# Kernel tuning notes

Measured on AMD Instinct MI355X. Metric: run time of the kernel, lower is better.

Reference implementation:

```python
import jax, jax.numpy as jnp
import numpy as np

N_NODES = 100000
NEG_SLOPE = 0.2


def gat_conv(x, edge_index, W, a_src, a_dst, bias):
    """PyG GATConv, heads=1, concat, add_self_loops=True."""
    N = x.shape[0]
    loop = jnp.arange(N, dtype=edge_index.dtype)
    src = jnp.concatenate([edge_index[0], loop])  # message sources j
    dst = jnp.concatenate([edge_index[1], loop])  # message targets i
    h = x @ W                                      # [N, out]
    asrc = h @ a_src                               # [N]
    adst = h @ a_dst                               # [N]
    e = jax.nn.leaky_relu(asrc[src] + adst[dst], NEG_SLOPE)   # [E+N]
    m = jax.ops.segment_max(e, dst, num_segments=N)           # per-dst max
    w = jnp.exp(e - jax.lax.stop_gradient(m)[dst])
    denom = jax.ops.segment_sum(w, dst, num_segments=N)
    alpha = w / denom[dst]                                     # softmax per dst
    out = jax.ops.segment_sum(alpha[:, None] * h[src], dst, num_segments=N)
    return out + bias


def setup_inputs() -> dict:
    key = jax.random.key(0)
    ks = jax.random.split(key, 16)
    N, E, D = N_NODES, 3200000, 128
    x = jax.random.normal(ks[0], (N, D), dtype=jnp.float32)
    edge_index = jax.random.randint(ks[1], (2, E), 0, N, dtype=jnp.int64)
    def glorot(k, shape):
        fan = sum(shape)
        return jax.random.uniform(k, shape, jnp.float32, -1.0, 1.0) * np.sqrt(6.0 / fan)
    return {
        "x": x,
        "edge_index": edge_index,
        "W1": glorot(ks[2], (D, 16)),
        "a1_src": glorot(ks[3], (16,)),
        "a1_dst": glorot(ks[4], (16,)),
        "b1": jnp.zeros((16,), jnp.float32),
        "W2": glorot(ks[5], (16, 10)),
        "a2_src": glorot(ks[6], (10,)),
        "a2_dst": glorot(ks[7], (10,)),
        "b2": jnp.zeros((10,), jnp.float32),
        "Wl1": glorot(ks[8], (10, 10)),
        "bl1": jnp.zeros((10,), jnp.float32),
        "Wl2": glorot(ks[9], (10, 1)),
        "bl2": jnp.zeros((1,), jnp.float32),
    }


def reference(x, edge_index, W1, a1_src, a1_dst, b1, W2, a2_src, a2_dst, b2,
              Wl1, bl1, Wl2, bl2):
    h = gat_conv(x, edge_index, W1, a1_src, a1_dst, b1)
    h = jax.nn.relu(h)
    h = gat_conv(h, edge_index, W2, a2_src, a2_dst, b2)
    h = h @ Wl1 + bl1
    h = jax.nn.relu(h)
    return h @ Wl2 + bl2  # [N, 1]
```

## Files before the change

kernel.cpp:

```cpp
#include <hip/hip_runtime.h>
#include <hip/hip_fp16.h>


#define NEG 0.2f
#define FSH 7
#define BNODES 128
#define NSBMAX 1024
#define CAPB 4608
#define TILE 4096
#define EPT 16
#define HN 64
#define SCAP 3072
#define PESA 18

__device__ __forceinline__ float lrelu(float x) { return x > 0.0f ? x : NEG * x; }

__device__ __forceinline__ unsigned fenc(float f) {
    unsigned u = __float_as_uint(f);
    return (u & 0x80000000u) ? ~u : (u | 0x80000000u);
}
__device__ __forceinline__ float fdec(unsigned e) {
    return (e & 0x80000000u) ? __uint_as_float(e & 0x7FFFFFFFu) : __uint_as_float(~e);
}

__device__ __forceinline__ float4 ldh4(const __half* h, size_t off) {
    uint2 u = *(const uint2*)(h + off);
    __half2 a = *(__half2*)&u.x, b = *(__half2*)&u.y;
    float2 fa = __half22float2(a), fb = __half22float2(b);
    return make_float4(fa.x, fa.y, fb.x, fb.y);
}

__global__ __launch_bounds__(256) void k_front(
    const float* __restrict__ x, const float* __restrict__ W1,
    const float* __restrict__ a1s, const float* __restrict__ a1d,
    __half* __restrict__ h1, float* __restrict__ s1, float* __restrict__ d1,
    unsigned* __restrict__ gmax,
    const int* __restrict__ esrc, const int* __restrict__ edst,
    int* __restrict__ bcur, unsigned* __restrict__ pairs,
    int N, int E, int NG, int NC, int NSB)
{
    __shared__ float smem[9220];
    int tid = threadIdx.x;
    int bid = blockIdx.x;
    long long T = (long long)NG + NC;
    int before = (int)(((long long)bid * NC) / T);
    int isc = (int)((((long long)bid + 1) * NC) / T) > before;

    if (isc) {
        unsigned* lsrt = (unsigned*)smem;
        int* lhist = (int*)smem + TILE;
        int* lofs  = lhist + NSBMAX;
        int* gbase = lofs + NSBMAX;
        int* wsum  = gbase + NSBMAX;
        unsigned short* rid = (unsigned short*)(smem + TILE + 3 * NSBMAX + 4);
        int cid = before;
        int base = cid * TILE;
        int tcnt = min(TILE, E - base);
        for (int i = tid; i < NSB; i += 256) lhist[i] = 0;
        __syncthreads();
        int ed[EPT];
#pragma unroll
        for (int u = 0; u < EPT; ++u) {
            int i = tid + u * 256;
            ed[u] = (i < tcnt) ? edst[base + i] : -1;
            if (ed[u] >= 0) atomicAdd(&lhist[ed[u] >> FSH], 1);
        }
        __syncthreads();
        int i0 = 4 * tid;
        int a0 = (i0 + 0 < NSB) ? lhist[i0 + 0] : 0;
        int a1 = (i0 + 1 < NSB) ? lhist[i0 + 1] : 0;
        int a2 = (i0 + 2 < NSB) ? lhist[i0 + 2] : 0;
        int a3 = (i0 + 3 < NSB) ? lhist[i0 + 3] : 0;
        int s = a0 + a1 + a2 + a3, pfx = s;
#pragma unroll
        for (int off = 1; off < 64; off <<= 1) {
            int t = __shfl_up(pfx, off, 64);
            if ((tid & 63) >= off) pfx += t;
        }
        if ((tid & 63) == 63) wsum[tid >> 6] = pfx;
        __syncthreads();
        int carry = 0;
        for (int w = 0; w < (tid >> 6); ++w) carry += wsum[w];
        int excl = pfx + carry - s;
        if (i0 + 0 < NSB) { lofs[i0 + 0] = excl;                 gbase[i0 + 0] = a0 ? atomicAdd(&bcur[(i0 + 0) * 16], a0) : 0; }
        if (i0 + 1 < NSB) { lofs[i0 + 1] = excl + a0;            gbase[i0 + 1] = a1 ? atomicAdd(&bcur[(i0 + 1) * 16], a1) : 0; }
        if (i0 + 2 < NSB) { lofs[i0 + 2] = excl + a0 + a1;       gbase[i0 + 2] = a2 ? atomicAdd(&bcur[(i0 + 2) * 16], a2) : 0; }
        if (i0 + 3 < NSB) { lofs[i0 + 3] = excl + a0 + a1 + a2;  gbase[i0 + 3] = a3 ? atomicAdd(&bcur[(i0 + 3) * 16], a3) : 0; }
        __syncthreads();
        if (i0 + 0 < NSB) lhist[i0 + 0] = lofs[i0 + 0];
        if (i0 + 1 < NSB) lhist[i0 + 1] = lofs[i0 + 1];
        if (i0 + 2 < NSB) lhist[i0 + 2] = lofs[i0 + 2];
        if (i0 + 3 < NSB) lhist[i0 + 3] = lofs[i0 + 3];
        __syncthreads();
#pragma unroll
        for (int u = 0; u < EPT; ++u) {
            int i = tid + u * 256;
            if (ed[u] >= 0) {
                int d = ed[u], srcv = esrc[base + i];
                int b = d >> FSH;
                int pos = atomicAdd(&lhist[b], 1);
                lsrt[pos] = ((unsigned)(d & (BNODES - 1)) << 17) | (unsigned)srcv;
                rid[pos] = (unsigned short)b;
            }
        }
        __syncthreads();
        for (int i = tid; i < tcnt; i += 256) {
            int r = rid[i];
            int rel = gbase[r] + (i - lofs[r]);
            if (rel < CAPB) pairs[(size_t)r * CAPB + rel] = lsrt[i];
        }
        return;
    }

    float* sW = smem;
    float* wm = smem + 2060;
    int gid = bid - before;
    for (int i = tid; i < 2048; i += 256) sW[i + ((i >> 9) << 2)] = W1[i];
    int node0 = gid * 64;
    int node = node0 + (tid >> 2);
    int q = tid & 3;
    bool valid = node < N;
    float4 xr[8];
    {
        const float4* xp = (const float4*)x + (size_t)node * 32 + q * 8;
#pragma unroll
        for (int k = 0; k < 8; ++k)
            xr[k] = valid ? xp[k] : make_float4(0.f, 0.f, 0.f, 0.f);
    }
    __syncthreads();

    float acc[16];
#pragma unroll
    for (int c = 0; c < 16; ++c) acc[c] = 0.f;
    int wbase = q * 516;
#pragma unroll
    for (int k = 0; k < 8; ++k) {
        float xs0 = xr[k].x, xs1 = xr[k].y, xs2 = xr[k].z, xs3 = xr[k].w;
#pragma unroll
        for (int t = 0; t < 4; ++t) {
            float xv = (t == 0) ? xs0 : (t == 1) ? xs1 : (t == 2) ? xs2 : xs3;
            const float4* wrow = (const float4*)&sW[wbase + (k * 4 + t) * 16];
            float4 w0 = wrow[0], w1 = wrow[1], w2 = wrow[2], w3 = wrow[3];
            acc[0]  += xv * w0.x; acc[1]  += xv * w0.y; acc[2]  += xv * w0.z; acc[3]  += xv * w0.w;
            acc[4]  += xv * w1.x; acc[5]  += xv * w1.y; acc[6]  += xv * w1.z; acc[7]  += xv * w1.w;
            acc[8]  += xv * w2.x; acc[9]  += xv * w2.y; acc[10] += xv * w2.z; acc[11] += xv * w2.w;
            acc[12] += xv * w3.x; acc[13] += xv * w3.y; acc[14] += xv * w3.z; acc[15] += xv * w3.w;
        }
    }
#pragma unroll
    for (int c = 0; c < 16; ++c) {
        acc[c] += __shfl_xor(acc[c], 1);
        acc[c] += __shfl_xor(acc[c], 2);
    }
    float sv = 0.f, dv = 0.f;
    {
        const float4* asp = (const float4*)a1s;
        const float4* adp = (const float4*)a1d;
#pragma unroll
        for (int r = 0; r < 4; ++r) {
            float4 as = asp[r], ad = adp[r];
            sv += acc[r*4+0]*as.x + acc[r*4+1]*as.y + acc[r*4+2]*as.z + acc[r*4+3]*as.w;
            dv += acc[r*4+0]*ad.x + acc[r*4+1]*ad.y + acc[r*4+2]*ad.z + acc[r*4+3]*ad.w;
        }
    }
    if (valid) {
        float4 av;
        if      (q == 0) av = make_float4(acc[0],  acc[1],  acc[2],  acc[3]);
        else if (q == 1) av = make_float4(acc[4],  acc[5],  acc[6],  acc[7]);
        else if (q == 2) av = make_float4(acc[8],  acc[9],  acc[10], acc[11]);
        else             av = make_float4(acc[12], acc[13], acc[14], acc[15]);
        __half2 p0 = __floats2half2_rn(av.x, av.y);
        __half2 p1 = __floats2half2_rn(av.z, av.w);
        uint2 u; u.x = *(unsigned*)&p0; u.y = *(unsigned*)&p1;
        *(uint2*)&h1[(size_t)node * 16 + q * 4] = u;
        if (q == 0) { s1[node] = sv; d1[node] = dv; }
    }
    float m = valid ? sv : -3.4e38f;
#pragma unroll
    for (int off = 32; off >= 1; off >>= 1) m = fmaxf(m, __shfl_xor(m, off));
    if ((tid & 63) == 0) wm[tid >> 6] = m;
    __syncthreads();
    if (tid == 0) {
        float b = fmaxf(fmaxf(wm[0], wm[1]), fmaxf(wm[2], wm[3]));
        atomicMax(gmax, fenc(b));
    }
}

__global__ __launch_bounds__(256) void k_agg1(
    const int* __restrict__ bcur, const unsigned* __restrict__ pairs,
    const int* __restrict__ esrc, const int* __restrict__ edst,
    const float* __restrict__ s1, const float* __restrict__ d1, const __half* __restrict__ h1,
    const float* __restrict__ b1, const float* __restrict__ W2,
    const float* __restrict__ a2s, const float* __restrict__ a2d,
    __half* __restrict__ h2, float* __restrict__ s2, float* __restrict__ d2,
    const unsigned* __restrict__ gmax1p, unsigned* __restrict__ gmax2, int N, int E)
{
    __shared__ unsigned srt[SCAP];
    __shared__ float accs[HN * 17];
    __shared__ int lcnt[HN];
    __shared__ int lofs[HN + 1];
    __shared__ float dds[HN], mbs[HN];
    __shared__ float sW[160], sb[16], sas[16], sad[16];
    __shared__ float wm[4];

    int tid = threadIdx.x;
    int fb = blockIdx.x >> 1;
    int hf = blockIdx.x & 1;
    int node0 = blockIdx.x << 6;
    if (tid < 160) sW[tid] = W2[tid];
    if (tid < 16) {
        sb[tid]  = b1[tid];
        sas[tid] = (tid < 10) ? a2s[tid] : 0.f;
        sad[tid] = (tid < 10) ? a2d[tid] : 0.f;
    }
    float g0 = fdec(*gmax1p);
    if (tid < HN) {
        int n = node0 + tid;
        float dd = (n < N) ? d1[n] : 0.f;
        dds[tid] = dd; mbs[tid] = lrelu(g0 + dd);
        lcnt[tid] = 0;
    }
    __syncthreads();

    int rbase = fb * CAPB;
    int cnt = bcur[fb * 16];
    int gg = tid >> 2, q = tid & 3;

    bool ok = (cnt <= CAPB);
    unsigned pe[PESA];
    if (ok) {
#pragma unroll
        for (int u = 0; u < PESA; ++u) {
            int i = tid + u * 256;
            bool v = (i < cnt);
            pe[u] = v ? pairs[rbase + i] : 0u;
            if (v) {
                int dl = (pe[u] >> 17) & (BNODES - 1);
                if ((dl >> 6) == hf) atomicAdd(&lcnt[dl & (HN - 1)], 1);
            }
        }
        __syncthreads();
        if (tid < HN) {
            int c = lcnt[tid];
            int pfx = c;
#pragma unroll
            for (int off = 1; off < 64; off <<= 1) {
                int t = __shfl_up(pfx, off, 64);
                if (tid >= off) pfx += t;
            }
            lofs[tid + 1] = pfx;
            lcnt[tid] = pfx - c;
            if (tid == 0) lofs[0] = 0;
        }
        __syncthreads();
        if (lofs[HN] > SCAP) ok = false;
    }

    if (ok) {
#pragma unroll
        for (int u = 0; u < PESA; ++u) {
            int i = tid + u * 256;
            if (i < cnt) {
                unsigned p = pe[u];
                int dl = (p >> 17) & (BNODES - 1);
                if ((dl >> 6) == hf) {
                    int pos = atomicAdd(&lcnt[dl & (HN - 1)], 1);
                    srt[pos] = p & 0x1FFFF;
                }
            }
        }
        __syncthreads();

        int n = node0 + gg;
        float4 accv; float den;
        if (n < N) {
            float w = __expf(lrelu(s1[n] + dds[gg]) - mbs[gg]);
            float4 hv = ldh4(h1, (size_t)n * 16 + 4 * q);
            accv = make_float4(w * hv.x, w * hv.y, w * hv.z, w * hv.w);
            den = w;
        } else { accv = make_float4(0.f, 0.f, 0.f, 0.f); den = 0.f; }
        {
            float dd = dds[gg], mb = mbs[gg];
            int j = lofs[gg], j1 = lofs[gg + 1];
            for (; j + 4 <= j1; j += 4) {
                int e0 = srt[j], e1 = srt[j + 1], e2 = srt[j + 2], e3 = srt[j + 3];
                float4 H0 = ldh4(h1, (size_t)e0 * 16 + 4 * q);
                float4 H1 = ldh4(h1, (size_t)e1 * 16 + 4 * q);
                float4 H2 = ldh4(h1, (size_t)e2 * 16 + 4 * q);
                float4 H3 = ldh4(h1, (size_t)e3 * 16 + 4 * q);
                int eq = srt[j + q];
                float wq = __expf(lrelu(s1[eq] + dd) - mb);
                float w0 = __shfl(wq, 0, 4), w1 = __shfl(wq, 1, 4);
                float w2 = __shfl(wq, 2, 4), w3 = __shfl(wq, 3, 4);
                accv.x += w0 * H0.x + w1 * H1.x + w2 * H2.x + w3 * H3.x;
                accv.y += w0 * H0.y + w1 * H1.y + w2 * H2.y + w3 * H3.y;
                accv.z += w0 * H0.z + w1 * H1.z + w2 * H2.z + w3 * H3.z;
                accv.w += w0 * H0.w + w1 * H1.w + w2 * H2.w + w3 * H3.w;
                den += (w0 + w1) + (w2 + w3);
            }
            for (; j < j1; ++j) {
                int e0 = srt[j];
                float w0 = __expf(lrelu(s1[e0] + dd) - mb);
                float4 H0 = ldh4(h1, (size_t)e0 * 16 + 4 * q);
                accv.x += w0 * H0.x; accv.y += w0 * H0.y;
                accv.z += w0 * H0.z; accv.w += w0 * H0.w;
                den += w0;
            }
        }
        accs[gg * 17 + 4 * q + 0] = accv.x;
        accs[gg * 17 + 4 * q + 1] = accv.y;
        accs[gg * 17 + 4 * q + 2] = accv.z;
        accs[gg * 17 + 4 * q + 3] = accv.w;
        if (q == 0) accs[gg * 17 + 16] = den;
        __syncthreads();
    } else {
        for (int i = tid; i < HN * 17; i += 256) accs[i] = 0.f;
        __syncthreads();
        if (tid < HN) {
            int n = node0 + tid;
            if (n < N) {
                float w = __expf(lrelu(s1[n] + dds[tid]) - mbs[tid]);
#pragma unroll
                for (int t = 0; t < 16; ++t)
                    accs[tid * 17 + t] = w * __half2float(h1[(size_t)n * 16 + t]);
                accs[tid * 17 + 16] = w;
            }
        }
        __syncthreads();
        for (int i = tid; i < E; i += 256) {
            int d = edst[i];
            if ((d >> 6) != blockIdx.x) continue;
            int nl = d & (HN - 1), src = esrc[i];
            float w = __expf(lrelu(s1[src] + dds[nl]) - mbs[nl]);
#pragma unroll
            for (int t = 0; t < 16; ++t)
                atomicAdd(&accs[nl * 17 + t], w * __half2float(h1[(size_t)src * 16 + t]));
            atomicAdd(&accs[nl * 17 + 16], w);
        }
        __syncthreads();
    }

    int g = tid >> 4, k = tid & 15;
    float sval = -3.4e38f;
#pragma unroll
    for (int qq = 0; qq < 4; ++qq) {
        int nl = g * 4 + qq, nn = node0 + nl;
        if (nn >= N) continue;
        float inv = 1.f / accs[nl * 17 + 16];
        float o = fmaxf(accs[nl * 17 + k] * inv + sb[k], 0.f);
        float hh = 0.f;
#pragma unroll
        for (int kk = 0; kk < 16; ++kk) {
            float ov = __shfl(o, kk, 16);
            if (k < 10) hh += ov * sW[kk * 10 + k];
        }
        if (k >= 10) hh = 0.f;
        float ts = hh * sas[k];
        float td = hh * sad[k];
#pragma unroll
        for (int off = 1; off < 16; off <<= 1) {
            ts += __shfl_xor(ts, off, 16);
            td += __shfl_xor(td, off, 16);
        }
        h2[(size_t)nn * 16 + k] = __float2half_rn(hh);
        if (k == 0) { s2[nn] = ts; d2[nn] = td; }
        sval = fmaxf(sval, ts);
    }
    float m = sval;
#pragma unroll
    for (int off = 32; off >= 1; off >>= 1) m = fmaxf(m, __shfl_xor(m, off));
    if ((tid & 63) == 0) wm[tid >> 6] = m;
    __syncthreads();
    if (tid == 0) {
        float bmx = fmaxf(fmaxf(wm[0], wm[1]), fmaxf(wm[2], wm[3]));
        atomicMax(gmax2, fenc(bmx));
    }
}

__global__ __launch_bounds__(256) void k_agg2(
    const int* __restrict__ bcur, const unsigned* __restrict__ pairs,
    const int* __restrict__ esrc, const int* __restrict__ edst,
    const float* __restrict__ s2, const float* __restrict__ d2, const __half* __restrict__ h2,
    const float* __restrict__ b2, const float* __restrict__ Wl1, const float* __restrict__ bl1,
    const float* __restrict__ Wl2, const float* __restrict__ bl2,
    const unsigned* __restrict__ gmax2p, float* __restrict__ out, int N, int E)
{
    __shared__ unsigned srt[SCAP];
    __shared__ float accs[HN * 17];
    __shared__ int lcnt[HN];
    __shared__ int lofs[HN + 1];
    __shared__ float dds[HN], mbs[HN];
    __shared__ float sW1[100], sb1[16], sW2[16], sb2g[16];
    __shared__ float sbl2;

    int tid = threadIdx.x;
    int fb = blockIdx.x >> 1;
    int hf = blockIdx.x & 1;
    int node0 = blockIdx.x << 6;
    if (tid < 100) sW1[tid] = Wl1[tid];
    if (tid < 16) {
        sb1[tid]  = (tid < 10) ? bl1[tid] : 0.f;
        sW2[tid]  = (tid < 10) ? Wl2[tid] : 0.f;
        sb2g[tid] = (tid < 10) ? b2[tid]  : 0.f;
    }
    if (tid == 0) sbl2 = bl2[0];
    float g0 = fdec(*gmax2p);
    if (tid < HN) {
        int n = node0 + tid;
        float dd = (n < N) ? d2[n] : 0.f;
        dds[tid] = dd; mbs[tid] = lrelu(g0 + dd);
        lcnt[tid] = 0;
    }
    __syncthreads();

    int rbase = fb * CAPB;
    int cnt = bcur[fb * 16];
    int gg = tid >> 2, q = tid & 3;

    bool ok = (cnt <= CAPB);
    unsigned pe[PESA];
    if (ok) {
#pragma unroll
        for (int u = 0; u < PESA; ++u) {
            int i = tid + u * 256;
            bool v = (i < cnt);
            pe[u] = v ? pairs[rbase + i] : 0u;
            if (v) {
                int dl = (pe[u] >> 17) & (BNODES - 1);
                if ((dl >> 6) == hf) atomicAdd(&lcnt[dl & (HN - 1)], 1);
            }
        }
        __syncthreads();
        if (tid < HN) {
            int c = lcnt[tid];
            int pfx = c;
#pragma unroll
            for (int off = 1; off < 64; off <<= 1) {
                int t = __shfl_up(pfx, off, 64);
                if (tid >= off) pfx += t;
            }
            lofs[tid + 1] = pfx;
            lcnt[tid] = pfx - c;
            if (tid == 0) lofs[0] = 0;
        }
        __syncthreads();
        if (lofs[HN] > SCAP) ok = false;
    }

    if (ok) {
#pragma unroll
        for (int u = 0; u < PESA; ++u) {
            int i = tid + u * 256;
            if (i < cnt) {
                unsigned p = pe[u];
                int dl = (p >> 17) & (BNODES - 1);
                if ((dl >> 6) == hf) {
                    int pos = atomicAdd(&lcnt[dl & (HN - 1)], 1);
                    srt[pos] = p & 0x1FFFF;
                }
            }
        }
        __syncthreads();

        int n = node0 + gg;
        float4 accv; float den;
        if (n < N) {
            float w = __expf(lrelu(s2[n] + dds[gg]) - mbs[gg]);
            float4 hv = ldh4(h2, (size_t)n * 16 + 4 * q);
            accv = make_float4(w * hv.x, w * hv.y, w * hv.z, w * hv.w);
            den = w;
        } else { accv = make_float4(0.f, 0.f, 0.f, 0.f); den = 0.f; }
        {
            float dd = dds[gg], mb = mbs[gg];
            int j = lofs[gg], j1 = lofs[gg + 1];
            for (; j + 4 <= j1; j += 4) {
                int e0 = srt[j], e1 = srt[j + 1], e2 = srt[j + 2], e3 = srt[j + 3];
                float4 H0 = ldh4(h2, (size_t)e0 * 16 + 4 * q);
                float4 H1 = ldh4(h2, (size_t)e1 * 16 + 4 * q);
                float4 H2 = ldh4(h2, (size_t)e2 * 16 + 4 * q);
                float4 H3 = ldh4(h2, (size_t)e3 * 16 + 4 * q);
                int eq = srt[j + q];
                float wq = __expf(lrelu(s2[eq] + dd) - mb);
                float w0 = __shfl(wq, 0, 4), w1 = __shfl(wq, 1, 4);
                float w2 = __shfl(wq, 2, 4), w3 = __shfl(wq, 3, 4);
                accv.x += w0 * H0.x + w1 * H1.x + w2 * H2.x + w3 * H3.x;
                accv.y += w0 * H0.y + w1 * H1.y + w2 * H2.y + w3 * H3.y;
                accv.z += w0 * H0.z + w1 * H1.z + w2 * H2.z + w3 * H3.z;
                accv.w += w0 * H0.w + w1 * H1.w + w2 * H2.w + w3 * H3.w;
                den += (w0 + w1) + (w2 + w3);
            }
            for (; j < j1; ++j) {
                int e0 = srt[j];
                float w0 = __expf(lrelu(s2[e0] + dd) - mb);
                float4 H0 = ldh4(h2, (size_t)e0 * 16 + 4 * q);
                accv.x += w0 * H0.x; accv.y += w0 * H0.y;
                accv.z += w0 * H0.z; accv.w += w0 * H0.w;
                den += w0;
            }
        }
        accs[gg * 17 + 4 * q + 0] = accv.x;
        accs[gg * 17 + 4 * q + 1] = accv.y;
        accs[gg * 17 + 4 * q + 2] = accv.z;
        accs[gg * 17 + 4 * q + 3] = accv.w;
        if (q == 0) accs[gg * 17 + 16] = den;
        __syncthreads();
    } else {
        for (int i = tid; i < HN * 17; i += 256) accs[i] = 0.f;
        __syncthreads();
        if (tid < HN) {
            int n = node0 + tid;
            if (n < N) {
                float w = __expf(lrelu(s2[n] + dds[tid]) - mbs[tid]);
#pragma unroll
                for (int t = 0; t < 16; ++t)
                    accs[tid * 17 + t] = w * __half2float(h2[(size_t)n * 16 + t]);
                accs[tid * 17 + 16] = w;
            }
        }
        __syncthreads();
        for (int i = tid; i < E; i += 256) {
            int d = edst[i];
            if ((d >> 6) != blockIdx.x) continue;
            int nl = d & (HN - 1), src = esrc[i];
            float w = __expf(lrelu(s2[src] + dds[nl]) - mbs[nl]);
#pragma unroll
            for (int t = 0; t < 16; ++t)
                atomicAdd(&accs[nl * 17 + t], w * __half2float(h2[(size_t)src * 16 + t]));
            atomicAdd(&accs[nl * 17 + 16], w);
        }
        __syncthreads();
    }

    int g = tid >> 4, k = tid & 15;
    bool fk = k < 10;
#pragma unroll
    for (int qq = 0; qq < 4; ++qq) {
        int nl = g * 4 + qq, nn = node0 + nl;
        if (nn >= N) continue;
        float inv = 1.f / accs[nl * 17 + 16];
        float o = fk ? accs[nl * 17 + k] * inv + sb2g[k] : 0.f;
        float v = sb1[k];
#pragma unroll
        for (int kk = 0; kk < 10; ++kk) {
            float ov = __shfl(o, kk, 16);
            if (fk) v += ov * sW1[kk * 10 + k];
        }
        float t = fmaxf(v, 0.f);
        float cc = t * sW2[k];
#pragma unroll
        for (int off = 1; off < 16; off <<= 1) cc += __shfl_xor(cc, off, 16);
        if (k == 0) out[nn] = cc + sbl2;
    }
}

extern "C" void kernel_launch(void* const* d_in, const int* in_sizes, int n_in,
                              void* d_out, int out_size, void* d_ws, size_t ws_size,
                              hipStream_t stream)
{
    const float* x   = (const float*)d_in[0];
    const int*   ei  = (const int*)  d_in[1];
    const float* W1  = (const float*)d_in[2];
    const float* a1s = (const float*)d_in[3];
    const float* a1d = (const float*)d_in[4];
    const float* b1  = (const float*)d_in[5];
    const float* W2  = (const float*)d_in[6];
    const float* a2s = (const float*)d_in[7];
    const float* a2d = (const float*)d_in[8];
    const float* b2  = (const float*)d_in[9];
    const float* Wl1 = (const float*)d_in[10];
    const float* bl1 = (const float*)d_in[11];
    const float* Wl2 = (const float*)d_in[12];
    const float* bl2 = (const float*)d_in[13];

    int N = in_sizes[0] / 128;
    int E = in_sizes[1] / 2;
    const int* ei_src = ei;
    const int* ei_dst = ei + E;
    int NSB = (N + BNODES - 1) >> FSH;

    size_t Np = ((size_t)N + 3) & ~(size_t)3;
    size_t need_bytes = (16 + (size_t)NSB * 16) * 4 + Np * 20 * 4 + (size_t)NSB * CAPB * 4;
    if (ws_size < need_bytes) return;

    unsigned* gmax1 = (unsigned*)d_ws;
    unsigned* gmax2 = gmax1 + 1;
    int* bcur = (int*)d_ws + 16;
    float* rest = (float*)d_ws + 16 + (size_t)NSB * 16;
    __half* h1 = (__half*)rest;
    float* s1 = rest + Np * 8;
    float* d1 = s1 + Np;
    __half* h2 = (__half*)(d1 + Np);
    float* s2 = (float*)(h2) + Np * 8;
    float* d2 = s2 + Np;
    unsigned* pairs = (unsigned*)(d2 + Np);

    int NG = (N + 63) / 64;
    int NC = (E + TILE - 1) / TILE;

    hipMemsetAsync(d_ws, 0, (16 + (size_t)NSB * 16) * sizeof(int), stream);
    hipLaunchKernelGGL(k_front, dim3(NG + NC), dim3(256), 0, stream,
                       x, W1, a1s, a1d, h1, s1, d1, gmax1,
                       ei_src, ei_dst, bcur, pairs, N, E, NG, NC, NSB);
    hipLaunchKernelGGL(k_agg1, dim3(NSB * 2), dim3(256), 0, stream,
                       bcur, pairs, ei_src, ei_dst, s1, d1, h1, b1, W2, a2s, a2d,
                       h2, s2, d2, gmax1, gmax2, N, E);
    hipLaunchKernelGGL(k_agg2, dim3(NSB * 2), dim3(256), 0, stream,
                       bcur, pairs, ei_src, ei_dst, s2, d2, h2, b2, Wl1, bl1, Wl2, bl2,
                       gmax2, (float*)d_out, N, E);
}
```

Before: 276.5 us.

## Fuse both aggregation kernels into one cooperative kernel with grid sync

Merges the layer-1 and layer-2 aggregation kernels into a single cooperative launch that sorts each block's edge bucket into shared memory once and reuses it for both layers. A grid-wide sync replaces the kernel boundary, so the global max for layer 2 is read after all blocks have contributed. This removes one launch, the second pass over the pair buckets and their re-sort. The cost is that all 1564 blocks must be co-resident (launch bounds of 7 blocks per CU), which limits registers. If that occupancy check fails, the original two kernels run instead.

```diff
diff --git a/kernel.cpp b/kernel.cpp
--- a/kernel.cpp
+++ b/kernel.cpp
@@ -1,5 +1,8 @@
 #include <hip/hip_runtime.h>
 #include <hip/hip_fp16.h>
+#include <hip/hip_cooperative_groups.h>
+
+namespace cg = cooperative_groups;
 
 
 #define NEG 0.2f
@@ -186,14 +189,17 @@
     }
 }
 
-__global__ __launch_bounds__(256) void k_agg1(
+__global__ __launch_bounds__(256, 7) void k_aggf(
     const int* __restrict__ bcur, const unsigned* __restrict__ pairs,
     const int* __restrict__ esrc, const int* __restrict__ edst,
     const float* __restrict__ s1, const float* __restrict__ d1, const __half* __restrict__ h1,
     const float* __restrict__ b1, const float* __restrict__ W2,
     const float* __restrict__ a2s, const float* __restrict__ a2d,
     __half* __restrict__ h2, float* __restrict__ s2, float* __restrict__ d2,
-    const unsigned* __restrict__ gmax1p, unsigned* __restrict__ gmax2, int N, int E)
+    const unsigned* __restrict__ gmax1p, unsigned* __restrict__ gmax2,
+    const float* __restrict__ b2, const float* __restrict__ Wl1, const float* __restrict__ bl1,
+    const float* __restrict__ Wl2, const float* __restrict__ bl2,
+    float* __restrict__ out, int N, int E)
 {
     __shared__ unsigned srt[SCAP];
     __shared__ float accs[HN * 17];
@@ -201,18 +207,26 @@
     __shared__ int lofs[HN + 1];
     __shared__ float dds[HN], mbs[HN];
     __shared__ float sW[160], sb[16], sas[16], sad[16];
+    __shared__ float sW1[100], sb1[16], sW2[16], sb2g[16];
+    __shared__ float sbl2;
     __shared__ float wm[4];
+    __shared__ int s_ok;
 
     int tid = threadIdx.x;
     int fb = blockIdx.x >> 1;
     int hf = blockIdx.x & 1;
     int node0 = blockIdx.x << 6;
     if (tid < 160) sW[tid] = W2[tid];
+    if (tid < 100) sW1[tid] = Wl1[tid];
     if (tid < 16) {
-        sb[tid]  = b1[tid];
-        sas[tid] = (tid < 10) ? a2s[tid] : 0.f;
-        sad[tid] = (tid < 10) ? a2d[tid] : 0.f;
-    }
+        sb[tid]   = b1[tid];
+        sas[tid]  = (tid < 10) ? a2s[tid] : 0.f;
+        sad[tid]  = (tid < 10) ? a2d[tid] : 0.f;
+        sb1[tid]  = (tid < 10) ? bl1[tid] : 0.f;
+        sW2[tid]  = (tid < 10) ? Wl2[tid] : 0.f;
+        sb2g[tid] = (tid < 10) ? b2[tid]  : 0.f;
+    }
+    if (tid == 0) sbl2 = bl2[0];
     float g0 = fdec(*gmax1p);
     if (tid < HN) {
         int n = node0 + tid;
@@ -227,8 +241,8 @@
     int gg = tid >> 2, q = tid & 3;
 
     bool ok = (cnt <= CAPB);
-    unsigned pe[PESA];
     if (ok) {
+        unsigned pe[PESA];
 #pragma unroll
         for (int u = 0; u < PESA; ++u) {
             int i = tid + u * 256;
@@ -254,23 +268,25 @@
         }
         __syncthreads();
         if (lofs[HN] > SCAP) ok = false;
-    }
-
-    if (ok) {
-#pragma unroll
-        for (int u = 0; u < PESA; ++u) {
-            int i = tid + u * 256;
-            if (i < cnt) {
-                unsigned p = pe[u];
-                int dl = (p >> 17) & (BNODES - 1);
-                if ((dl >> 6) == hf) {
-                    int pos = atomicAdd(&lcnt[dl & (HN - 1)], 1);
-                    srt[pos] = p & 0x1FFFF;
+        if (ok) {
+#pragma unroll
+            for (int u = 0; u < PESA; ++u) {
+                int i = tid + u * 256;
+                if (i < cnt) {
+                    unsigned p = pe[u];
+                    int dl = (p >> 17) & (BNODES - 1);
+                    if ((dl >> 6) == hf) {
+                        int pos = atomicAdd(&lcnt[dl & (HN - 1)], 1);
+                        srt[pos] = p & 0x1FFFF;
+                    }
                 }
             }
         }
-        __syncthreads();
-
+    }
+    if (tid == 0) s_ok = ok ? 1 : 0;
+    __syncthreads();
+
+    if (s_ok) {
         int n = node0 + gg;
         float4 accv; float den;
         if (n < N) {
@@ -340,128 +356,55 @@
         __syncthreads();
     }
 
-    int g = tid >> 4, k = tid & 15;
-    float sval = -3.4e38f;
-#pragma unroll
-    for (int qq = 0; qq < 4; ++qq) {
-        int nl = g * 4 + qq, nn = node0 + nl;
-        if (nn >= N) continue;
-        float inv = 1.f / accs[nl * 17 + 16];
-        float o = fmaxf(accs[nl * 17 + k] * inv + sb[k], 0.f);
-        float hh = 0.f;
-#pragma unroll
-        for (int kk = 0; kk < 16; ++kk) {
-            float ov = __shfl(o, kk, 16);
-            if (k < 10) hh += ov * sW[kk * 10 + k];
-        }
-        if (k >= 10) hh = 0.f;
-        float ts = hh * sas[k];
-        float td = hh * sad[k];
-#pragma unroll
-        for (int off = 1; off < 16; off <<= 1) {
-            ts += __shfl_xor(ts, off, 16);
-            td += __shfl_xor(td, off, 16);
-        }
-        h2[(size_t)nn * 16 + k] = __float2half_rn(hh);
-        if (k == 0) { s2[nn] = ts; d2[nn] = td; }
-        sval = fmaxf(sval, ts);
-    }
-    float m = sval;
-#pragma unroll
-    for (int off = 32; off >= 1; off >>= 1) m = fmaxf(m, __shfl_xor(m, off));
-    if ((tid & 63) == 0) wm[tid >> 6] = m;
-    __syncthreads();
-    if (tid == 0) {
-        float bmx = fmaxf(fmaxf(wm[0], wm[1]), fmaxf(wm[2], wm[3]));
-        atomicMax(gmax2, fenc(bmx));
-    }
-}
-
-__global__ __launch_bounds__(256) void k_agg2(
-    const int* __restrict__ bcur, const unsigned* __restrict__ pairs,
-    const int* __restrict__ esrc, const int* __restrict__ edst,
-    const float* __restrict__ s2, const float* __restrict__ d2, const __half* __restrict__ h2,
-    const float* __restrict__ b2, const float* __restrict__ Wl1, const float* __restrict__ bl1,
-    const float* __restrict__ Wl2, const float* __restrict__ bl2,
-    const unsigned* __restrict__ gmax2p, float* __restrict__ out, int N, int E)
-{
-    __shared__ unsigned srt[SCAP];
-    __shared__ float accs[HN * 17];
-    __shared__ int lcnt[HN];
-    __shared__ int lofs[HN + 1];
-    __shared__ float dds[HN], mbs[HN];
-    __shared__ float sW1[100], sb1[16], sW2[16], sb2g[16];
-    __shared__ float sbl2;
-
-    int tid = threadIdx.x;
-    int fb = blockIdx.x >> 1;
-    int hf = blockIdx.x & 1;
-    int node0 = blockIdx.x << 6;
-    if (tid < 100) sW1[tid] = Wl1[tid];
-    if (tid < 16) {
-        sb1[tid]  = (tid < 10) ? bl1[tid] : 0.f;
-        sW2[tid]  = (tid < 10) ? Wl2[tid] : 0.f;
-        sb2g[tid] = (tid < 10) ? b2[tid]  : 0.f;
-    }
-    if (tid == 0) sbl2 = bl2[0];
-    float g0 = fdec(*gmax2p);
+    {
+        int g = tid >> 4, k = tid & 15;
+        float sval = -3.4e38f;
+#pragma unroll
+        for (int qq = 0; qq < 4; ++qq) {
+            int nl = g * 4 + qq, nn = node0 + nl;
+            if (nn >= N) continue;
+            float inv = 1.f / accs[nl * 17 + 16];
+            float o = fmaxf(accs[nl * 17 + k] * inv + sb[k], 0.f);
+            float hh = 0.f;
+#pragma unroll
+            for (int kk = 0; kk < 16; ++kk) {
+                float ov = __shfl(o, kk, 16);
+                if (k < 10) hh += ov * sW[kk * 10 + k];
+            }
+            if (k >= 10) hh = 0.f;
+            float ts = hh * sas[k];
+            float td = hh * sad[k];
+#pragma unroll
+            for (int off = 1; off < 16; off <<= 1) {
+                ts += __shfl_xor(ts, off, 16);
+                td += __shfl_xor(td, off, 16);
+            }
+            h2[(size_t)nn * 16 + k] = __float2half_rn(hh);
+            if (k == 0) { s2[nn] = ts; d2[nn] = td; }
+            sval = fmaxf(sval, ts);
+        }
+        float m = sval;
+#pragma unroll
+        for (int off = 32; off >= 1; off >>= 1) m = fmaxf(m, __shfl_xor(m, off));
+        if ((tid & 63) == 0) wm[tid >> 6] = m;
+        __syncthreads();
+        if (tid == 0) {
+            float bmx = fmaxf(fmaxf(wm[0], wm[1]), fmaxf(wm[2], wm[3]));
+            atomicMax(gmax2, fenc(bmx));
+        }
+    }
+
+    cg::this_grid().sync();
+
+    float g2 = fdec(*(const volatile unsigned*)gmax2);
     if (tid < HN) {
         int n = node0 + tid;
         float dd = (n < N) ? d2[n] : 0.f;
-        dds[tid] = dd; mbs[tid] = lrelu(g0 + dd);
-        lcnt[tid] = 0;
+        dds[tid] = dd; mbs[tid] = lrelu(g2 + dd);
     }
     __syncthreads();
 
-    int rbase = fb * CAPB;
-    int cnt = bcur[fb * 16];
-    int gg = tid >> 2, q = tid & 3;
-
-    bool ok = (cnt <= CAPB);
-    unsigned pe[PESA];
-    if (ok) {
-#pragma unroll
-        for (int u = 0; u < PESA; ++u) {
-            int i = tid + u * 256;
-            bool v = (i < cnt);
-            pe[u] = v ? pairs[rbase + i] : 0u;
-            if (v) {
-                int dl = (pe[u] >> 17) & (BNODES - 1);
-                if ((dl >> 6) == hf) atomicAdd(&lcnt[dl & (HN - 1)], 1);
-            }
-        }
-        __syncthreads();
-        if (tid < HN) {
-            int c = lcnt[tid];
-            int pfx = c;
-#pragma unroll
-            for (int off = 1; off < 64; off <<= 1) {
-                int t = __shfl_up(pfx, off, 64);
-                if (tid >= off) pfx += t;
-            }
-            lofs[tid + 1] = pfx;
-            lcnt[tid] = pfx - c;
-            if (tid == 0) lofs[0] = 0;
-        }
-        __syncthreads();
-        if (lofs[HN] > SCAP) ok = false;
-    }
-
-    if (ok) {
-#pragma unroll
-        for (int u = 0; u < PESA; ++u) {
-            int i = tid + u * 256;
-            if (i < cnt) {
-                unsigned p = pe[u];
-                int dl = (p >> 17) & (BNODES - 1);
-                if ((dl >> 6) == hf) {
-                    int pos = atomicAdd(&lcnt[dl & (HN - 1)], 1);
-                    srt[pos] = p & 0x1FFFF;
-                }
-            }
-        }
-        __syncthreads();
-
+    if (s_ok) {
         int n = node0 + gg;
         float4 accv; float den;
         if (n < N) {
@@ -498,6 +441,376 @@
                 den += w0;
             }
         }
+        __syncthreads();
+        accs[gg * 17 + 4 * q + 0] = accv.x;
+        accs[gg * 17 + 4 * q + 1] = accv.y;
+        accs[gg * 17 + 4 * q + 2] = accv.z;
+        accs[gg * 17 + 4 * q + 3] = accv.w;
+        if (q == 0) accs[gg * 17 + 16] = den;
+        __syncthreads();
+    } else {
+        for (int i = tid; i < HN * 17; i += 256) accs[i] = 0.f;
+        __syncthreads();
+        if (tid < HN) {
+            int n = node0 + tid;
+            if (n < N) {
+                float w = __expf(lrelu(s2[n] + dds[tid]) - mbs[tid]);
+#pragma unroll
+                for (int t = 0; t < 16; ++t)
+                    accs[tid * 17 + t] = w * __half2float(h2[(size_t)n * 16 + t]);
+                accs[tid * 17 + 16] = w;
+            }
+        }
+        __syncthreads();
+        for (int i = tid; i < E; i += 256) {
+            int d = edst[i];
+            if ((d >> 6) != blockIdx.x) continue;
+            int nl = d & (HN - 1), src = esrc[i];
+            float w = __expf(lrelu(s2[src] + dds[nl]) - mbs[nl]);
+#pragma unroll
+            for (int t = 0; t < 16; ++t)
+                atomicAdd(&accs[nl * 17 + t], w * __half2float(h2[(size_t)src * 16 + t]));
+            atomicAdd(&accs[nl * 17 + 16], w);
+        }
+        __syncthreads();
+    }
+
+    {
+        int g = tid >> 4, k = tid & 15;
+        bool fk = k < 10;
+#pragma unroll
+        for (int qq = 0; qq < 4; ++qq) {
+            int nl = g * 4 + qq, nn = node0 + nl;
+            if (nn >= N) continue;
+            float inv = 1.f / accs[nl * 17 + 16];
+            float o = fk ? accs[nl * 17 + k] * inv + sb2g[k] : 0.f;
+            float v = sb1[k];
+#pragma unroll
+            for (int kk = 0; kk < 10; ++kk) {
+                float ov = __shfl(o, kk, 16);
+                if (fk) v += ov * sW1[kk * 10 + k];
+            }
+            float t = fmaxf(v, 0.f);
+            float cc = t * sW2[k];
+#pragma unroll
+            for (int off = 1; off < 16; off <<= 1) cc += __shfl_xor(cc, off, 16);
+            if (k == 0) out[nn] = cc + sbl2;
+        }
+    }
+}
+
+__global__ __launch_bounds__(256) void k_agg1(
+    const int* __restrict__ bcur, const unsigned* __restrict__ pairs,
+    const int* __restrict__ esrc, const int* __restrict__ edst,
+    const float* __restrict__ s1, const float* __restrict__ d1, const __half* __restrict__ h1,
+    const float* __restrict__ b1, const float* __restrict__ W2,
+    const float* __restrict__ a2s, const float* __restrict__ a2d,
+    __half* __restrict__ h2, float* __restrict__ s2, float* __restrict__ d2,
+    const unsigned* __restrict__ gmax1p, unsigned* __restrict__ gmax2, int N, int E)
+{
+    __shared__ unsigned srt[SCAP];
+    __shared__ float accs[HN * 17];
+    __shared__ int lcnt[HN];
+    __shared__ int lofs[HN + 1];
+    __shared__ float dds[HN], mbs[HN];
+    __shared__ float sW[160], sb[16], sas[16], sad[16];
+    __shared__ float wm[4];
+
+    int tid = threadIdx.x;
+    int fb = blockIdx.x >> 1;
+    int hf = blockIdx.x & 1;
+    int node0 = blockIdx.x << 6;
+    if (tid < 160) sW[tid] = W2[tid];
+    if (tid < 16) {
+        sb[tid]  = b1[tid];
+        sas[tid] = (tid < 10) ? a2s[tid] : 0.f;
+        sad[tid] = (tid < 10) ? a2d[tid] : 0.f;
+    }
+    float g0 = fdec(*gmax1p);
+    if (tid < HN) {
+        int n = node0 + tid;
+        float dd = (n < N) ? d1[n] : 0.f;
+        dds[tid] = dd; mbs[tid] = lrelu(g0 + dd);
+        lcnt[tid] = 0;
+    }
+    __syncthreads();
+
+    int rbase = fb * CAPB;
+    int cnt = bcur[fb * 16];
+    int gg = tid >> 2, q = tid & 3;
+
+    bool ok = (cnt <= CAPB);
+    unsigned pe[PESA];
+    if (ok) {
+#pragma unroll
+        for (int u = 0; u < PESA; ++u) {
+            int i = tid + u * 256;
+            bool v = (i < cnt);
+            pe[u] = v ? pairs[rbase + i] : 0u;
+            if (v) {
+                int dl = (pe[u] >> 17) & (BNODES - 1);
+                if ((dl >> 6) == hf) atomicAdd(&lcnt[dl & (HN - 1)], 1);
+            }
+        }
+        __syncthreads();
+        if (tid < HN) {
+            int c = lcnt[tid];
+            int pfx = c;
+#pragma unroll
+            for (int off = 1; off < 64; off <<= 1) {
+                int t = __shfl_up(pfx, off, 64);
+                if (tid >= off) pfx += t;
+            }
+            lofs[tid + 1] = pfx;
+            lcnt[tid] = pfx - c;
+            if (tid == 0) lofs[0] = 0;
+        }
+        __syncthreads();
+        if (lofs[HN] > SCAP) ok = false;
+    }
+
+    if (ok) {
+#pragma unroll
+        for (int u = 0; u < PESA; ++u) {
+            int i = tid + u * 256;
+            if (i < cnt) {
+                unsigned p = pe[u];
+                int dl = (p >> 17) & (BNODES - 1);
+                if ((dl >> 6) == hf) {
+                    int pos = atomicAdd(&lcnt[dl & (HN - 1)], 1);
+                    srt[pos] = p & 0x1FFFF;
+                }
+            }
+        }
+        __syncthreads();
+
+        int n = node0 + gg;
+        float4 accv; float den;
+        if (n < N) {
+            float w = __expf(lrelu(s1[n] + dds[gg]) - mbs[gg]);
+            float4 hv = ldh4(h1, (size_t)n * 16 + 4 * q);
+            accv = make_float4(w * hv.x, w * hv.y, w * hv.z, w * hv.w);
+            den = w;
+        } else { accv = make_float4(0.f, 0.f, 0.f, 0.f); den = 0.f; }
+        {
+            float dd = dds[gg], mb = mbs[gg];
+            int j = lofs[gg], j1 = lofs[gg + 1];
+            for (; j + 4 <= j1; j += 4) {
+                int e0 = srt[j], e1 = srt[j + 1], e2 = srt[j + 2], e3 = srt[j + 3];
+                float4 H0 = ldh4(h1, (size_t)e0 * 16 + 4 * q);
+                float4 H1 = ldh4(h1, (size_t)e1 * 16 + 4 * q);
+                float4 H2 = ldh4(h1, (size_t)e2 * 16 + 4 * q);
+                float4 H3 = ldh4(h1, (size_t)e3 * 16 + 4 * q);
+                int eq = srt[j + q];
+                float wq = __expf(lrelu(s1[eq] + dd) - mb);
+                float w0 = __shfl(wq, 0, 4), w1 = __shfl(wq, 1, 4);
+                float w2 = __shfl(wq, 2, 4), w3 = __shfl(wq, 3, 4);
+                accv.x += w0 * H0.x + w1 * H1.x + w2 * H2.x + w3 * H3.x;
+                accv.y += w0 * H0.y + w1 * H1.y + w2 * H2.y + w3 * H3.y;
+                accv.z += w0 * H0.z + w1 * H1.z + w2 * H2.z + w3 * H3.z;
+                accv.w += w0 * H0.w + w1 * H1.w + w2 * H2.w + w3 * H3.w;
+                den += (w0 + w1) + (w2 + w3);
+            }
+            for (; j < j1; ++j) {
+                int e0 = srt[j];
+                float w0 = __expf(lrelu(s1[e0] + dd) - mb);
+                float4 H0 = ldh4(h1, (size_t)e0 * 16 + 4 * q);
+                accv.x += w0 * H0.x; accv.y += w0 * H0.y;
+                accv.z += w0 * H0.z; accv.w += w0 * H0.w;
+                den += w0;
+            }
+        }
+        accs[gg * 17 + 4 * q + 0] = accv.x;
+        accs[gg * 17 + 4 * q + 1] = accv.y;
+        accs[gg * 17 + 4 * q + 2] = accv.z;
+        accs[gg * 17 + 4 * q + 3] = accv.w;
+        if (q == 0) accs[gg * 17 + 16] = den;
+        __syncthreads();
+    } else {
+        for (int i = tid; i < HN * 17; i += 256) accs[i] = 0.f;
+        __syncthreads();
+        if (tid < HN) {
+            int n = node0 + tid;
+            if (n < N) {
+                float w = __expf(lrelu(s1[n] + dds[tid]) - mbs[tid]);
+#pragma unroll
+                for (int t = 0; t < 16; ++t)
+                    accs[tid * 17 + t] = w * __half2float(h1[(size_t)n * 16 + t]);
+                accs[tid * 17 + 16] = w;
+            }
+        }
+        __syncthreads();
+        for (int i = tid; i < E; i += 256) {
+            int d = edst[i];
+            if ((d >> 6) != blockIdx.x) continue;
+            int nl = d & (HN - 1), src = esrc[i];
+            float w = __expf(lrelu(s1[src] + dds[nl]) - mbs[nl]);
+#pragma unroll
+            for (int t = 0; t < 16; ++t)
+                atomicAdd(&accs[nl * 17 + t], w * __half2float(h1[(size_t)src * 16 + t]));
+            atomicAdd(&accs[nl * 17 + 16], w);
+        }
+        __syncthreads();
+    }
+
+    int g = tid >> 4, k = tid & 15;
+    float sval = -3.4e38f;
+#pragma unroll
+    for (int qq = 0; qq < 4; ++qq) {
+        int nl = g * 4 + qq, nn = node0 + nl;
+        if (nn >= N) continue;
+        float inv = 1.f / accs[nl * 17 + 16];
+        float o = fmaxf(accs[nl * 17 + k] * inv + sb[k], 0.f);
+        float hh = 0.f;
+#pragma unroll
+        for (int kk = 0; kk < 16; ++kk) {
+            float ov = __shfl(o, kk, 16);
+            if (k < 10) hh += ov * sW[kk * 10 + k];
+        }
+        if (k >= 10) hh = 0.f;
+        float ts = hh * sas[k];
+        float td = hh * sad[k];
+#pragma unroll
+        for (int off = 1; off < 16; off <<= 1) {
+            ts += __shfl_xor(ts, off, 16);
+            td += __shfl_xor(td, off, 16);
+        }
+        h2[(size_t)nn * 16 + k] = __float2half_rn(hh);
+        if (k == 0) { s2[nn] = ts; d2[nn] = td; }
+        sval = fmaxf(sval, ts);
+    }
+    float m = sval;
+#pragma unroll
+    for (int off = 32; off >= 1; off >>= 1) m = fmaxf(m, __shfl_xor(m, off));
+    if ((tid & 63) == 0) wm[tid >> 6] = m;
+    __syncthreads();
+    if (tid == 0) {
+        float bmx = fmaxf(fmaxf(wm[0], wm[1]), fmaxf(wm[2], wm[3]));
+        atomicMax(gmax2, fenc(bmx));
+    }
+}
+
+__global__ __launch_bounds__(256) void k_agg2(
+    const int* __restrict__ bcur, const unsigned* __restrict__ pairs,
+    const int* __restrict__ esrc, const int* __restrict__ edst,
+    const float* __restrict__ s2, const float* __restrict__ d2, const __half* __restrict__ h2,
+    const float* __restrict__ b2, const float* __restrict__ Wl1, const float* __restrict__ bl1,
+    const float* __restrict__ Wl2, const float* __restrict__ bl2,
+    const unsigned* __restrict__ gmax2p, float* __restrict__ out, int N, int E)
+{
+    __shared__ unsigned srt[SCAP];
+    __shared__ float accs[HN * 17];
+    __shared__ int lcnt[HN];
+    __shared__ int lofs[HN + 1];
+    __shared__ float dds[HN], mbs[HN];
+    __shared__ float sW1[100], sb1[16], sW2[16], sb2g[16];
+    __shared__ float sbl2;
+
+    int tid = threadIdx.x;
+    int fb = blockIdx.x >> 1;
+    int hf = blockIdx.x & 1;
+    int node0 = blockIdx.x << 6;
+    if (tid < 100) sW1[tid] = Wl1[tid];
+    if (tid < 16) {
+        sb1[tid]  = (tid < 10) ? bl1[tid] : 0.f;
+        sW2[tid]  = (tid < 10) ? Wl2[tid] : 0.f;
+        sb2g[tid] = (tid < 10) ? b2[tid]  : 0.f;
+    }
+    if (tid == 0) sbl2 = bl2[0];
+    float g0 = fdec(*gmax2p);
+    if (tid < HN) {
+        int n = node0 + tid;
+        float dd = (n < N) ? d2[n] : 0.f;
+        dds[tid] = dd; mbs[tid] = lrelu(g0 + dd);
+        lcnt[tid] = 0;
+    }
+    __syncthreads();
+
+    int rbase = fb * CAPB;
+    int cnt = bcur[fb * 16];
+    int gg = tid >> 2, q = tid & 3;
+
+    bool ok = (cnt <= CAPB);
+    unsigned pe[PESA];
+    if (ok) {
+#pragma unroll
+        for (int u = 0; u < PESA; ++u) {
+            int i = tid + u * 256;
+            bool v = (i < cnt);
+            pe[u] = v ? pairs[rbase + i] : 0u;
+            if (v) {
+                int dl = (pe[u] >> 17) & (BNODES - 1);
+                if ((dl >> 6) == hf) atomicAdd(&lcnt[dl & (HN - 1)], 1);
+            }
+        }
+        __syncthreads();
+        if (tid < HN) {
+            int c = lcnt[tid];
+            int pfx = c;
+#pragma unroll
+            for (int off = 1; off < 64; off <<= 1) {
+                int t = __shfl_up(pfx, off, 64);
+                if (tid >= off) pfx += t;
+            }
+            lofs[tid + 1] = pfx;
+            lcnt[tid] = pfx - c;
+            if (tid == 0) lofs[0] = 0;
+        }
+        __syncthreads();
+        if (lofs[HN] > SCAP) ok = false;
+    }
+
+    if (ok) {
+#pragma unroll
+        for (int u = 0; u < PESA; ++u) {
+            int i = tid + u * 256;
+            if (i < cnt) {
+                unsigned p = pe[u];
+                int dl = (p >> 17) & (BNODES - 1);
+                if ((dl >> 6) == hf) {
+                    int pos = atomicAdd(&lcnt[dl & (HN - 1)], 1);
+                    srt[pos] = p & 0x1FFFF;
+                }
+            }
+        }
+        __syncthreads();
+
+        int n = node0 + gg;
+        float4 accv; float den;
+        if (n < N) {
+            float w = __expf(lrelu(s2[n] + dds[gg]) - mbs[gg]);
+            float4 hv = ldh4(h2, (size_t)n * 16 + 4 * q);
+            accv = make_float4(w * hv.x, w * hv.y, w * hv.z, w * hv.w);
+            den = w;
+        } else { accv = make_float4(0.f, 0.f, 0.f, 0.f); den = 0.f; }
+        {
+            float dd = dds[gg], mb = mbs[gg];
+            int j = lofs[gg], j1 = lofs[gg + 1];
+            for (; j + 4 <= j1; j += 4) {
+                int e0 = srt[j], e1 = srt[j + 1], e2 = srt[j + 2], e3 = srt[j + 3];
+                float4 H0 = ldh4(h2, (size_t)e0 * 16 + 4 * q);
+                float4 H1 = ldh4(h2, (size_t)e1 * 16 + 4 * q);
+                float4 H2 = ldh4(h2, (size_t)e2 * 16 + 4 * q);
+                float4 H3 = ldh4(h2, (size_t)e3 * 16 + 4 * q);
+                int eq = srt[j + q];
+                float wq = __expf(lrelu(s2[eq] + dd) - mb);
+                float w0 = __shfl(wq, 0, 4), w1 = __shfl(wq, 1, 4);
+                float w2 = __shfl(wq, 2, 4), w3 = __shfl(wq, 3, 4);
+                accv.x += w0 * H0.x + w1 * H1.x + w2 * H2.x + w3 * H3.x;
+                accv.y += w0 * H0.y + w1 * H1.y + w2 * H2.y + w3 * H3.y;
+                accv.z += w0 * H0.z + w1 * H1.z + w2 * H2.z + w3 * H3.z;
+                accv.w += w0 * H0.w + w1 * H1.w + w2 * H2.w + w3 * H3.w;
+                den += (w0 + w1) + (w2 + w3);
+            }
+            for (; j < j1; ++j) {
+                int e0 = srt[j];
+                float w0 = __expf(lrelu(s2[e0] + dd) - mb);
+                float4 H0 = ldh4(h2, (size_t)e0 * 16 + 4 * q);
+                accv.x += w0 * H0.x; accv.y += w0 * H0.y;
+                accv.z += w0 * H0.z; accv.w += w0 * H0.w;
+                den += w0;
+            }
+        }
         accs[gg * 17 + 4 * q + 0] = accv.x;
         accs[gg * 17 + 4 * q + 1] = accv.y;
         accs[gg * 17 + 4 * q + 2] = accv.z;
@@ -593,18 +906,51 @@
     float* s2 = (float*)(h2) + Np * 8;
     float* d2 = s2 + Np;
     unsigned* pairs = (unsigned*)(d2 + Np);
+    float* outp = (float*)d_out;
 
     int NG = (N + 63) / 64;
     int NC = (E + TILE - 1) / TILE;
+    int NHB = NSB * 2;
 
     hipMemsetAsync(d_ws, 0, (16 + (size_t)NSB * 16) * sizeof(int), stream);
     hipLaunchKernelGGL(k_front, dim3(NG + NC), dim3(256), 0, stream,
                        x, W1, a1s, a1d, h1, s1, d1, gmax1,
                        ei_src, ei_dst, bcur, pairs, N, E, NG, NC, NSB);
-    hipLaunchKernelGGL(k_agg1, dim3(NSB * 2), dim3(256), 0, stream,
-                       bcur, pairs, ei_src, ei_dst, s1, d1, h1, b1, W2, a2s, a2d,
-                       h2, s2, d2, gmax1, gmax2, N, E);
-    hipLaunchKernelGGL(k_agg2, dim3(NSB * 2), dim3(256), 0, stream,
-                       bcur, pairs, ei_src, ei_dst, s2, d2, h2, b2, Wl1, bl1, Wl2, bl2,
-                       gmax2, (float*)d_out, N, E);
+
+    bool coop = false;
+    {
+        int maxB = 0;
+        if (hipOccupancyMaxActiveBlocksPerMultiprocessor(&maxB, k_aggf, 256, 0) == hipSuccess) {
+            int dev = 0, nCU = 0;
+            hipGetDevice(&dev);
+            hipDeviceGetAttribute(&nCU, hipDeviceAttributeMultiprocessorCount, dev);
+            if (maxB > 0 && nCU > 0 && (long long)maxB * nCU >= (long long)NHB) coop = true;
+        }
+    }
+    if (coop) {
+        const int*      a_bcur = bcur;   const unsigned* a_pairs = pairs;
+        const int*      a_src  = ei_src; const int*      a_dst   = ei_dst;
+        const float*    a_s1 = s1; const float* a_d1 = d1; const __half* a_h1 = h1;
+        const unsigned* a_g1 = gmax1;
+        void* args[] = {
+            (void*)&a_bcur, (void*)&a_pairs, (void*)&a_src, (void*)&a_dst,
+            (void*)&a_s1, (void*)&a_d1, (void*)&a_h1,
+            (void*)&b1, (void*)&W2, (void*)&a2s, (void*)&a2d,
+            (void*)&h2, (void*)&s2, (void*)&d2,
+            (void*)&a_g1, (void*)&gmax2,
+            (void*)&b2, (void*)&Wl1, (void*)&bl1, (void*)&Wl2, (void*)&bl2,
+            (void*)&outp, (void*)&N, (void*)&E
+        };
+        hipError_t e = hipLaunchCooperativeKernel((const void*)k_aggf, dim3(NHB), dim3(256),
+                                                  args, 0, stream);
+        if (e != hipSuccess) coop = false;
+    }
+    if (!coop) {
+        hipLaunchKernelGGL(k_agg1, dim3(NHB), dim3(256), 0, stream,
+                           bcur, pairs, ei_src, ei_dst, s1, d1, h1, b1, W2, a2s, a2d,
+                           h2, s2, d2, gmax1, gmax2, N, E);
+        hipLaunchKernelGGL(k_agg2, dim3(NHB), dim3(256), 0, stream,
+                           bcur, pairs, ei_src, ei_dst, s2, d2, h2, b2, Wl1, bl1, Wl2, bl2,
+                           gmax2, (float*)d_out, N, E);
+    }
 }
```

Measured after the change: 274.4 us. About the same (-0.8%).
